# Kernel tuning notes

Measured on AMD Instinct MI355X. Metric: run time of the kernel, lower is better.

## Reference

```python
import jax, jax.numpy as jnp
import numpy as np

B, N, F, H, R = 16, 64, 64, 4, 50
C = F * H  # n_coefficients = n_heads * hidden_features
CUTOFF = 5.0  # ExpNormalSmearing cutoff_upper (cutoff_lower = 0)


def _dense(k, fin, fout):
    s = 1.0 / np.sqrt(fin)
    return jax.random.uniform(k, (fin, fout), jnp.float32, -s, s)


def setup_inputs() -> dict:
    key = jax.random.key(0)
    ks = jax.random.split(key, 20)
    start = float(np.exp(-CUTOFF))
    return {
        "h": jax.random.normal(ks[0], (B, N, F), jnp.float32),
        "x": jax.random.normal(ks[1], (B, N, 3), jnp.float32),
        "v": jax.random.normal(ks[2], (B, N, 3), jnp.float32) * 0.1,
        # edge model (ContinuousFilterConvolutionWithConcatenation)
        "W_in": _dense(ks[3], 2 * F, R), "b_in": jnp.zeros((R,), jnp.float32),
        "rbf_means": jnp.linspace(start, 1.0, R).astype(jnp.float32),
        "rbf_betas": jnp.full((R,), (2.0 / R * (1.0 - start)) ** -2, jnp.float32),
        "W_e1": _dense(ks[4], 2 * F + R + 1, F), "b_e1": jnp.zeros((F,), jnp.float32),
        "W_e2": _dense(ks[5], F, F), "b_e2": jnp.zeros((F,), jnp.float32),
        # semantic attention
        "W_sem": _dense(ks[6], F, H), "b_sem": jnp.zeros((H,), jnp.float32),
        "log_gamma": -jnp.log(jnp.linspace(1.0, 5.0, H)).astype(jnp.float32),
        # spatial attention
        "W_xmix": _dense(ks[7], C, C),
        "W_post1": _dense(ks[8], C, F), "b_post1": jnp.zeros((F,), jnp.float32),
        "W_post2": _dense(ks[9], F, F), "b_post2": jnp.zeros((F,), jnp.float32),
        # node update
        "W_node1": _dense(ks[10], F + C + F, F), "b_node1": jnp.zeros((F,), jnp.float32),
        "W_node2": _dense(ks[11], F, F), "b_node2": jnp.zeros((F,), jnp.float32),
        # velocity update
        "W_vel1": _dense(ks[12], F, F), "b_vel1": jnp.zeros((F,), jnp.float32),
        "W_vel2": _dense(ks[13], F, 1),
        "W_vmix": _dense(ks[14], C, 1),
    }


def reference(h, x, v, W_in, b_in, rbf_means, rbf_betas, W_e1, b_e1, W_e2, b_e2,
              W_sem, b_sem, log_gamma, W_xmix, W_post1, b_post1, W_post2, b_post2,
              W_node1, b_node1, W_node2, b_node2, W_vel1, b_vel1, W_vel2, W_vmix):
    silu = jax.nn.silu
    n = h.shape[-2]
    # pairwise displacement x_j - x_i : (B, N, N, 3)
    x_minus_xt = x[..., None, :, :] - x[..., :, None, :]
    d = jnp.sqrt(jax.nn.relu((x_minus_xt ** 2).sum(-1, keepdims=True)) + 1e-5)  # (B,N,N,1)
    # pairwise node features [h_j, h_i] : (B, N, N, 2F)
    hj = jnp.broadcast_to(h[..., None, :, :], h.shape[:-2] + (n, n, h.shape[-1]))
    hi = jnp.broadcast_to(h[..., :, None, :], hj.shape)
    h_cat = jnp.concatenate([hj, hi], -1)
    # edge model: RBF-smeared continuous-filter conv with concatenation
    h_mid = h_cat @ W_in + b_in  # (B,N,N,R)
    cut = 0.5 * (jnp.cos(d * (jnp.pi / CUTOFF)) + 1.0) * (d < CUTOFF)
    rbf = cut * jnp.exp(-rbf_betas * (jnp.exp(-d) - rbf_means) ** 2)  # (B,N,N,R)
    h_e = jnp.concatenate([h_cat, rbf * h_mid, d], -1)
    h_e = silu(h_e @ W_e1 + b_e1) @ W_e2 + b_e2  # (B,N,N,F)
    # attentions, softmax over neighbor axis (-2), diagonal masked out
    eye = jnp.eye(n, dtype=h.dtype)[:, :, None]
    sem = jax.nn.celu(h_e @ W_sem + b_sem, alpha=2.0) - 1e5 * eye
    sem = jax.nn.softmax(sem, axis=-2)  # (B,N,N,H)
    euc = jax.nn.softmax(-(d + 1e5 * eye) * jnp.exp(log_gamma), axis=-2)  # (B,N,N,H)
    att = euc * sem
    att = att / att.sum(-2, keepdims=True)
    # per-head attention-weighted edge features, flattened (F outer, H inner)
    h_e_att = (h_e[..., :, None] * att[..., None, :]).reshape(att.shape[:-1] + (F * H,))
    # spatial attention on unit displacement vectors
    coeff = jnp.tanh(h_e_att @ W_xmix)  # (B,N,N,C)
    x_hat = x_minus_xt / (d + 1e-5)
    comb = x_hat[..., None, :] * coeff[..., None]  # (B,N,N,C,3)
    comb_sum = comb.mean(axis=-3)  # mean over neighbors -> (B,N,C,3)
    h_comb = (comb_sum ** 2).sum(-1)  # invariant squared norms (B,N,C)
    h_comb = silu(silu(h_comb @ W_post1 + b_post1) @ W_post2 + b_post2)
    # node update (residual)
    h_agg = h_e_att.sum(axis=-2)  # (B,N,C)
    h_out = h + silu(silu(jnp.concatenate([h, h_agg, h_comb], -1) @ W_node1 + b_node1) @ W_node2 + b_node2)
    # equivariant velocity / coordinate update
    delta_v = jnp.einsum('...ijcd,c->...id', comb, W_vmix[:, 0]) / n  # v_mixing + mean over j
    gate = 2.0 * jax.nn.sigmoid(silu(h_out @ W_vel1 + b_vel1) @ W_vel2)  # double_sigmoid, (B,N,1)
    v_out = delta_v + gate * v
    x_out = x + v_out
    return h_out, x_out, v_out
```

## Files before the change

### kernel.cpp

```cpp
#include <hip/hip_runtime.h>
#include <math.h>

#define NB 16
#define NN 64
#define NF 64
#define NH 4
#define NR 50
#define NC 256

typedef __attribute__((ext_vector_type(8))) short short8;
typedef __attribute__((ext_vector_type(4))) float f32x4;

#define WS_WE1R 0
#define WS_WE2  4096
#define WS_WX   9216
#define WS_PO1  74752
#define WS_NO1  91136
#define WS_PO2  115712
#define WS_NO2  119808
#define WS_VE1  123904
#define MID_F   64000
#define E1_F    (MID_F + 131072)
#define HAGG_F  (E1_F + 131072)
#define COMB_F  (HAGG_F + 262144)
#define BS2_F   (COMB_F + 786432)

__device__ __forceinline__ float siluf(float x) { return x / (1.f + __expf(-x)); }
__device__ __forceinline__ float tanhfast(float x) { return 1.f - 2.f / (__expf(2.f * x) + 1.f); }

__device__ __forceinline__ short f2bfs(float f) {
    __bf16 b = (__bf16)f;
    union { __bf16 b; short s; } u; u.b = b; return u.s;
}
__device__ __forceinline__ float bf1(ushort u) {
    union { unsigned u; float f; } c; c.u = ((unsigned)u) << 16; return c.f;
}
__device__ __forceinline__ float bflo(unsigned u) {
    union { unsigned u; float f; } c; c.u = u << 16; return c.f;
}
__device__ __forceinline__ float bfhi(unsigned u) {
    union { unsigned u; float f; } c; c.u = u & 0xFFFF0000u; return c.f;
}

__global__ __launch_bounds__(256)
void prep_kernel(const float* __restrict__ W_e1, const float* __restrict__ b_e1,
                 const float* __restrict__ W_e2, const float* __restrict__ b_e2,
                 const float* __restrict__ W_sem, const float* __restrict__ b_sem,
                 const float* __restrict__ W_xmix,
                 const float* __restrict__ W_post1, const float* __restrict__ W_node1,
                 const float* __restrict__ W_post2, const float* __restrict__ W_node2,
                 const float* __restrict__ W_vel1,
                 const float* __restrict__ h, const float* __restrict__ W_in,
                 const float* __restrict__ b_in,
                 short* __restrict__ wpack, float* __restrict__ mid,
                 float* __restrict__ e1, float* __restrict__ bs2)
{
    int blk = blockIdx.x, t = threadIdx.x;
    if (blk < 63) {
        int s = blk * 256 + t;
        if (s >= 16000) return;
        short8 val;
        if (s < 512) {
            int cl = s & 15, g = (s >> 4) & 3, q = s >> 6;
            int ks = q & 1, nt = q >> 1;
            int c = nt * 16 + cl, k0 = 32 * ks + 8 * g;
#pragma unroll
            for (int i = 0; i < 8; i++) {
                int kr = k0 + i;
                float f = (kr < 50) ? W_e1[(128 + kr) * NF + c] : (kr == 50 ? W_e1[178 * NF + c] : 0.f);
                val[i] = f2bfs(f);
            }
            *(short8*)(&wpack[WS_WE1R + s * 8]) = val;
        } else if (s < 1152) {
            int u = s - 512;
            int cl = u & 15, g = (u >> 4) & 3, q = u >> 6;
            int ks = q & 1, nt = q >> 1;
            int c = nt * 16 + cl, k0 = 32 * ks + 8 * g;
#pragma unroll
            for (int i = 0; i < 8; i++) {
                int k = k0 + i;
                float f;
                if (c < 64) f = W_e2[k * NF + c];
                else {
                    int cc = (c - 64) & 3;
                    f = 0.f;
                    for (int m = 0; m < 64; m++) f += W_e2[k * NF + m] * W_sem[m * NH + cc];
                }
                val[i] = f2bfs(f);
            }
            *(short8*)(&wpack[WS_WE2 + u * 8]) = val;
        } else if (s < 9344) {
            int u = s - 1152;
            int l2 = u & 63, ks = (u >> 6) & 1, hh = (u >> 7) & 3, ct = u >> 9;
            int lr2 = l2 & 15, lg2 = l2 >> 4;
            int c = ct * 16 + lr2, k0 = ks * 32 + lg2 * 8;
#pragma unroll
            for (int i = 0; i < 8; i++)
                val[i] = f2bfs(W_xmix[((k0 + i) * 4 + hh) * NC + c]);
            *(short8*)(&wpack[WS_WX + u * 8]) = val;
        } else if (s < 11392) {
            int u = s - 9344;
            int cl = u & 15, g = (u >> 4) & 3, q = u >> 6;
            int ks = q & 7, nt = q >> 3;
            int c = nt * 16 + cl, k0 = 32 * ks + 8 * g;
#pragma unroll
            for (int i = 0; i < 8; i++) val[i] = f2bfs(W_post1[(k0 + i) * NF + c]);
            *(short8*)(&wpack[WS_PO1 + u * 8]) = val;
        } else if (s < 14464) {
            int u = s - 11392;
            int cl = u & 15, g = (u >> 4) & 3, q = u >> 6;
            int ks = q % 12, nt = q / 12;
            int c = nt * 16 + cl, k0 = 32 * ks + 8 * g;
#pragma unroll
            for (int i = 0; i < 8; i++) val[i] = f2bfs(W_node1[(k0 + i) * NF + c]);
            *(short8*)(&wpack[WS_NO1 + u * 8]) = val;
        } else if (s < 14976) {
            int u = s - 14464;
            int cl = u & 15, g = (u >> 4) & 3, q = u >> 6;
            int ks = q & 1, nt = q >> 1;
            int c = nt * 16 + cl, k0 = 32 * ks + 8 * g;
#pragma unroll
            for (int i = 0; i < 8; i++) val[i] = f2bfs(W_post2[(k0 + i) * NF + c]);
            *(short8*)(&wpack[WS_PO2 + u * 8]) = val;
        } else if (s < 15488) {
            int u = s - 14976;
            int cl = u & 15, g = (u >> 4) & 3, q = u >> 6;
            int ks = q & 1, nt = q >> 1;
            int c = nt * 16 + cl, k0 = 32 * ks + 8 * g;
#pragma unroll
            for (int i = 0; i < 8; i++) val[i] = f2bfs(W_node2[(k0 + i) * NF + c]);
            *(short8*)(&wpack[WS_NO2 + u * 8]) = val;
        } else {
            int u = s - 15488;
            int cl = u & 15, g = (u >> 4) & 3, q = u >> 6;
            int ks = q & 1, nt = q >> 1;
            int c = nt * 16 + cl, k0 = 32 * ks + 8 * g;
#pragma unroll
            for (int i = 0; i < 8; i++) val[i] = f2bfs(W_vel1[(k0 + i) * NF + c]);
            *(short8*)(&wpack[WS_VE1 + u * 8]) = val;
        }
    } else if (blk == 63) {
        if (t < 4) {
            float acc = b_sem[t];
            for (int m = 0; m < 64; m++) acc += b_e2[m] * W_sem[m * NH + t];
            bs2[t] = acc;
        }
    } else {
        int node = blk - 64;
        __shared__ float s_hn[64];
        if (t < 64) s_hn[t] = h[node * NF + t];
        __syncthreads();
        if (t < 64) {
            float acc = 0.f;
#pragma unroll 8
            for (int k = 0; k < 64; k++) acc += s_hn[k] * W_e1[k * NF + t];
            e1[node * 128 + t] = acc;
        } else if (t < 128) {
            int f = t - 64;
            float acc = b_e1[f];
#pragma unroll 8
            for (int k = 0; k < 64; k++) acc += s_hn[k] * W_e1[(64 + k) * NF + f];
            e1[node * 128 + 64 + f] = acc;
        } else if (t < 178) {
            int r = t - 128;
            float acc = 0.f;
#pragma unroll 8
            for (int k = 0; k < 64; k++) acc += s_hn[k] * W_in[k * NR + r];
            mid[node * 128 + r] = acc;
        } else if (t >= 192 && t < 242) {
            int r = t - 192;
            float acc = b_in[r];
#pragma unroll 8
            for (int k = 0; k < 64; k++) acc += s_hn[k] * W_in[(64 + k) * NR + r];
            mid[node * 128 + 64 + r] = acc;
        }
    }
}

__global__ __launch_bounds__(256)
void sake_edge_kernel(
    const float* __restrict__ x,
    const float* __restrict__ mid, const float* __restrict__ e1,
    const float* __restrict__ rbf_means, const float* __restrict__ rbf_betas,
    const float* __restrict__ b_e2, const float* __restrict__ bs2,
    const float* __restrict__ log_gamma,
    const short* __restrict__ wpack,
    float* __restrict__ hagg_g, float* __restrict__ comb_g)
{
    const int bi = blockIdx.x;
    const int b  = bi >> 6;
    const int i  = bi & 63;
    const int t  = threadIdx.x;
    const int w  = t >> 6, l = t & 63, lr = l & 15, lg = l >> 4;

    __shared__ __align__(16) short s_A[16 * 64 * 8];
    __shared__ __align__(16) short s_he[64 * 72];
    __shared__ float s_xhat[256];
    __shared__ float s_att[256];
    __shared__ float s_midi[52];

    const short8* A8  = (const short8*)s_A;
    short8*       A8w = (short8*)s_A;
    const short8* We1p = (const short8*)(wpack + WS_WE1R);
    const short8* We2p = (const short8*)(wpack + WS_WE2);
    const short8* Wxp  = (const short8*)(wpack + WS_WX);

    if (t < 50) s_midi[t] = mid[(b * 64 + i) * 128 + 64 + t];
    if (t < 64) {
        int j = t;
        float dx = x[(b * NN + j) * 3 + 0] - x[(b * NN + i) * 3 + 0];
        float dy = x[(b * NN + j) * 3 + 1] - x[(b * NN + i) * 3 + 1];
        float dz = x[(b * NN + j) * 3 + 2] - x[(b * NN + i) * 3 + 2];
        float d2 = dx * dx + dy * dy + dz * dz;
        float d  = sqrtf(fmaxf(d2, 0.f) + 1e-5f);
        float inv = 1.f / (d + 1e-5f);
        s_xhat[j * 4 + 0] = dx * inv;
        s_xhat[j * 4 + 1] = dy * inv;
        s_xhat[j * 4 + 2] = dz * inv;
        s_xhat[j * 4 + 3] = d;
    }
    __syncthreads();

    const int fW = w * 16 + lr;
    const float* e1b = e1 + (size_t)b * 64 * 128;
    float e1i_v = e1b[i * 128 + 64 + fW];
    float e1v[4][4];
#pragma unroll
    for (int jt = 0; jt < 4; jt++)
#pragma unroll
        for (int r = 0; r < 4; r++)
            e1v[jt][r] = e1b[(jt * 16 + lg * 4 + r) * 128 + fW];
    float be2 = b_e2[fW];
    float gam = __expf(log_gamma[lr & 3]);
    float bsv = bs2[lr & 3];

    {
        int j = t & 63, p = t >> 6;
        float d = s_xhat[j * 4 + 3];
        float cut = 0.5f * (__cosf(d * 0.6283185307179586f) + 1.f) * (d < 5.f ? 1.f : 0.f);
        float emd = __expf(-d);
        const float* mj = mid + (size_t)(b * 64 + j) * 128;
#pragma unroll
        for (int q = 0; q < 2; q++) {
            int sl = 2 * p + q;
            short8 val;
#pragma unroll
            for (int e = 0; e < 8; e++) {
                int r = sl * 8 + e;
                float o;
                if (r < 50) {
                    float m = mj[r] + s_midi[r];
                    float df = emd - rbf_means[r];
                    o = cut * __expf(-rbf_betas[r] * df * df) * m;
                } else if (r == 50) o = d;
                else o = 0.f;
                val[e] = f2bfs(o);
            }
            A8w[sl * 64 + j] = val;
        }
    }
    __syncthreads();

    {
        f32x4 acc[4];
#pragma unroll
        for (int jt = 0; jt < 4; jt++)
#pragma unroll
            for (int r = 0; r < 4; r++) acc[jt][r] = e1v[jt][r] + e1i_v;
#pragma unroll
        for (int ks = 0; ks < 2; ks++) {
            short8 bb = We1p[(w * 2 + ks) * 64 + l];
#pragma unroll
            for (int jt = 0; jt < 4; jt++) {
                short8 aa = A8[(ks * 4 + lg) * 64 + jt * 16 + lr];
                acc[jt] = __builtin_amdgcn_mfma_f32_16x16x32_bf16(aa, bb, acc[jt], 0, 0, 0);
            }
        }
#pragma unroll
        for (int jt = 0; jt < 4; jt++)
#pragma unroll
            for (int r = 0; r < 4; r++) {
                int j = jt * 16 + lg * 4 + r;
                s_A[(((fW >> 3) + 8) * 64 + j) * 8 + (fW & 7)] = f2bfs(siluf(acc[jt][r]));
            }
        __syncthreads();
    }

    {
        f32x4 accE[4], accS[4];
#pragma unroll
        for (int jt = 0; jt < 4; jt++) {
            accE[jt][0] = 0.f; accE[jt][1] = 0.f; accE[jt][2] = 0.f; accE[jt][3] = 0.f;
            accS[jt][0] = 0.f; accS[jt][1] = 0.f; accS[jt][2] = 0.f; accS[jt][3] = 0.f;
        }
#pragma unroll
        for (int ks = 0; ks < 2; ks++) {
            short8 aa[4];
#pragma unroll
            for (int jt = 0; jt < 4; jt++) aa[jt] = A8[(8 + ks * 4 + lg) * 64 + jt * 16 + lr];
            short8 bb = We2p[(w * 2 + ks) * 64 + l];
#pragma unroll
            for (int jt = 0; jt < 4; jt++)
                accE[jt] = __builtin_amdgcn_mfma_f32_16x16x32_bf16(aa[jt], bb, accE[jt], 0, 0, 0);
            if (w == 0) {
                short8 bb2 = We2p[(8 + ks) * 64 + l];
#pragma unroll
                for (int jt = 0; jt < 4; jt++)
                    accS[jt] = __builtin_amdgcn_mfma_f32_16x16x32_bf16(aa[jt], bb2, accS[jt], 0, 0, 0);
            }
        }
#pragma unroll
        for (int jt = 0; jt < 4; jt++)
#pragma unroll
            for (int r = 0; r < 4; r++) {
                int j = jt * 16 + lg * 4 + r;
                s_he[j * 72 + fW] = f2bfs(accE[jt][r] + be2);
            }
        if (w == 0) {
            float cel[4][4], dj[4][4];
            float m1 = -1e30f, m2 = -1e30f;
#pragma unroll
            for (int jt = 0; jt < 4; jt++)
#pragma unroll
                for (int r = 0; r < 4; r++) {
                    int j = jt * 16 + lg * 4 + r;
                    float s = accS[jt][r] + bsv;
                    float c = fmaxf(s, 0.f) + fminf(0.f, 2.f * (__expf(0.5f * s) - 1.f));
                    float d = s_xhat[j * 4 + 3];
                    if (j == i) { c -= 1e5f; d += 1e5f; }
                    cel[jt][r] = c; dj[jt][r] = d;
                    m1 = fmaxf(m1, c);
                    m2 = fmaxf(m2, -d * gam);
                }
            m1 = fmaxf(m1, __shfl_xor(m1, 16)); m1 = fmaxf(m1, __shfl_xor(m1, 32));
            m2 = fmaxf(m2, __shfl_xor(m2, 16)); m2 = fmaxf(m2, __shfl_xor(m2, 32));
            float S1 = 0.f, S2 = 0.f;
#pragma unroll
            for (int jt = 0; jt < 4; jt++)
#pragma unroll
                for (int r = 0; r < 4; r++) {
                    float ev1 = __expf(cel[jt][r] - m1);
                    float ev2 = __expf(-dj[jt][r] * gam - m2);
                    cel[jt][r] = ev1; dj[jt][r] = ev2;
                    S1 += ev1; S2 += ev2;
                }
            S1 += __shfl_xor(S1, 16); S1 += __shfl_xor(S1, 32);
            S2 += __shfl_xor(S2, 16); S2 += __shfl_xor(S2, 32);
            float inv12 = 1.f / (S1 * S2);
            float at[4][4];
            float S3 = 0.f;
#pragma unroll
            for (int jt = 0; jt < 4; jt++)
#pragma unroll
                for (int r = 0; r < 4; r++) {
                    at[jt][r] = cel[jt][r] * dj[jt][r] * inv12;
                    S3 += at[jt][r];
                }
            S3 += __shfl_xor(S3, 16); S3 += __shfl_xor(S3, 32);
            float inv3 = 1.f / S3;
            if (lr < 4) {
#pragma unroll
                for (int jt = 0; jt < 4; jt++)
#pragma unroll
                    for (int r = 0; r < 4; r++) {
                        int j = jt * 16 + lg * 4 + r;
                        s_att[j * 4 + lr] = at[jt][r] * inv3;
                    }
            }
        }
        __syncthreads();
    }

    {
        int f2 = t >> 3, hh = (t >> 1) & 3, jh = t & 1;
        float a0 = 0.f, a1 = 0.f;
#pragma unroll 8
        for (int jj = 0; jj < 32; jj++) {
            int j = jh * 32 + jj;
            float at = s_att[j * 4 + hh];
            unsigned u = *(const unsigned*)(s_he + j * 72 + 2 * f2);
            a0 += bflo(u) * at;
            a1 += bfhi(u) * at;
        }
        a0 += __shfl_xor(a0, 1);
        a1 += __shfl_xor(a1, 1);
        if (!jh) {
            hagg_g[bi * 256 + (2 * f2) * 4 + hh]     = a0;
            hagg_g[bi * 256 + (2 * f2 + 1) * 4 + hh] = a1;
        }
    }

    {
        f32x4 acc[4][4];
#pragma unroll
        for (int jt = 0; jt < 4; jt++)
#pragma unroll
            for (int ct = 0; ct < 4; ct++) {
                acc[jt][ct][0] = 0.f; acc[jt][ct][1] = 0.f;
                acc[jt][ct][2] = 0.f; acc[jt][ct][3] = 0.f;
            }
#pragma unroll 1
        for (int h = 0; h < 4; h++) {
            float ah[4];
#pragma unroll
            for (int jt = 0; jt < 4; jt++) ah[jt] = s_att[(jt * 16 + lr) * 4 + h];
#pragma unroll
            for (int ks = 0; ks < 2; ks++) {
                short8 fr[4];
#pragma unroll
                for (int jt = 0; jt < 4; jt++) {
                    short8 he8 = *(const short8*)(s_he + (jt * 16 + lr) * 72 + ks * 32 + lg * 8);
                    short8 v;
#pragma unroll
                    for (int e = 0; e < 8; e++) v[e] = f2bfs(bf1((ushort)he8[e]) * ah[jt]);
                    fr[jt] = v;
                }
#pragma unroll
                for (int ct = 0; ct < 4; ct++) {
                    short8 bb = Wxp[(((w * 4 + ct) * 4 + h) * 2 + ks) * 64 + l];
#pragma unroll
                    for (int jt = 0; jt < 4; jt++)
                        acc[jt][ct] = __builtin_amdgcn_mfma_f32_16x16x32_bf16(fr[jt], bb, acc[jt][ct], 0, 0, 0);
                }
            }
        }
        float* cgb = comb_g + bi * 768;
#pragma unroll
        for (int ct = 0; ct < 4; ct++) {
            float p0 = 0.f, p1 = 0.f, p2 = 0.f;
#pragma unroll
            for (int jt = 0; jt < 4; jt++)
#pragma unroll
                for (int r = 0; r < 4; r++) {
                    int j = jt * 16 + lg * 4 + r;
                    float4 xh = *(const float4*)(s_xhat + j * 4);
                    float th = tanhfast(acc[jt][ct][r]);
                    p0 += xh.x * th;
                    p1 += xh.y * th;
                    p2 += xh.z * th;
                }
            p0 += __shfl_xor(p0, 16); p0 += __shfl_xor(p0, 32);
            p1 += __shfl_xor(p1, 16); p1 += __shfl_xor(p1, 32);
            p2 += __shfl_xor(p2, 16); p2 += __shfl_xor(p2, 32);
            if (lg == 0) {
                int c = (w * 4 + ct) * 16 + lr;
                cgb[c]       = p0 * (1.f / 64.f);
                cgb[256 + c] = p1 * (1.f / 64.f);
                cgb[512 + c] = p2 * (1.f / 64.f);
            }
        }
    }
}

__global__ __launch_bounds__(256)
void sake_tail_kernel(
    const float* __restrict__ h, const float* __restrict__ x, const float* __restrict__ v,
    const float* __restrict__ hagg_g, const float* __restrict__ comb_g,
    const float* __restrict__ b_post1, const float* __restrict__ b_post2,
    const float* __restrict__ b_node1, const float* __restrict__ b_node2,
    const float* __restrict__ b_vel1,
    const float* __restrict__ W_vel2, const float* __restrict__ W_vmix,
    const short* __restrict__ wpack,
    float* __restrict__ out_h, float* __restrict__ out_x, float* __restrict__ out_v)
{
    const int g0 = blockIdx.x * 16;
    const int t = threadIdx.x;
    const int w = t >> 6, l = t & 63, lr = l & 15, lg = l >> 4;

    __shared__ __align__(16) short s_Aa[88 * 16 * 8];
    __shared__ float s_wv[256];
    __shared__ float s_wv2[64];
    __shared__ float s_red[4][16];

    const short8* A8  = (const short8*)s_Aa;
    const short8* PO1p = (const short8*)(wpack + WS_PO1);
    const short8* NO1p = (const short8*)(wpack + WS_NO1);
    const short8* PO2p = (const short8*)(wpack + WS_PO2);
    const short8* NO2p = (const short8*)(wpack + WS_NO2);
    const short8* VE1p = (const short8*)(wpack + WS_VE1);

    {
        s_wv[t] = W_vmix[t];
        if (t < 64) s_wv2[t] = W_vel2[t];
        int n = t & 15, c0 = (t >> 4) * 16;
        const float* cg = comb_g + (g0 + n) * 768;
        const float* ha = hagg_g + (g0 + n) * 256;
#pragma unroll
        for (int cc = 0; cc < 16; cc++) {
            int c = c0 + cc;
            float v0 = cg[c], v1 = cg[256 + c], v2 = cg[512 + c];
            float hcp = v0 * v0 + v1 * v1 + v2 * v2;
            s_Aa[((c >> 3) * 16 + n) * 8 + (c & 7)] = f2bfs(hcp);
            s_Aa[((40 + (c >> 3)) * 16 + n) * 8 + (c & 7)] = f2bfs(ha[c]);
        }
        int f0 = (t >> 4) * 4;
#pragma unroll
        for (int ff = 0; ff < 4; ff++) {
            int f = f0 + ff;
            s_Aa[((32 + (f >> 3)) * 16 + n) * 8 + (f & 7)] = f2bfs(h[(g0 + n) * 64 + f]);
        }
    }
    __syncthreads();

    {
        f32x4 acc = {0.f, 0.f, 0.f, 0.f};
#pragma unroll
        for (int ks = 0; ks < 8; ks++) {
            short8 aa = A8[(ks * 4 + lg) * 16 + lr];
            short8 bb = PO1p[((w * 8 + ks) * 4 + lg) * 16 + lr];
            acc = __builtin_amdgcn_mfma_f32_16x16x32_bf16(aa, bb, acc, 0, 0, 0);
        }
        int f = w * 16 + lr;
        float bp = b_post1[f];
        __syncthreads();
#pragma unroll
        for (int r = 0; r < 4; r++) {
            int n = lg * 4 + r;
            s_Aa[((80 + (f >> 3)) * 16 + n) * 8 + (f & 7)] = f2bfs(siluf(acc[r] + bp));
        }
        __syncthreads();
    }
    {
        f32x4 acc = {0.f, 0.f, 0.f, 0.f};
#pragma unroll
        for (int ks = 0; ks < 2; ks++) {
            short8 aa = A8[((80 + ks * 4 + lg)) * 16 + lr];
            short8 bb = PO2p[((w * 2 + ks) * 4 + lg) * 16 + lr];
            acc = __builtin_amdgcn_mfma_f32_16x16x32_bf16(aa, bb, acc, 0, 0, 0);
        }
        int f = w * 16 + lr;
        float bp = b_post2[f];
#pragma unroll
        for (int r = 0; r < 4; r++) {
            int n = lg * 4 + r;
            s_Aa[((72 + (f >> 3)) * 16 + n) * 8 + (f & 7)] = f2bfs(siluf(acc[r] + bp));
        }
        __syncthreads();
    }
    {
        f32x4 acc = {0.f, 0.f, 0.f, 0.f};
#pragma unroll
        for (int ks = 0; ks < 12; ks++) {
            short8 aa = A8[((32 + ks * 4 + lg)) * 16 + lr];
            short8 bb = NO1p[((w * 12 + ks) * 4 + lg) * 16 + lr];
            acc = __builtin_amdgcn_mfma_f32_16x16x32_bf16(aa, bb, acc, 0, 0, 0);
        }
        int f = w * 16 + lr;
        float bp = b_node1[f];
#pragma unroll
        for (int r = 0; r < 4; r++) {
            int n = lg * 4 + r;
            s_Aa[((f >> 3) * 16 + n) * 8 + (f & 7)] = f2bfs(siluf(acc[r] + bp));
        }
        __syncthreads();
    }
    {
        f32x4 acc = {0.f, 0.f, 0.f, 0.f};
#pragma unroll
        for (int ks = 0; ks < 2; ks++) {
            short8 aa = A8[(ks * 4 + lg) * 16 + lr];
            short8 bb = NO2p[((w * 2 + ks) * 4 + lg) * 16 + lr];
            acc = __builtin_amdgcn_mfma_f32_16x16x32_bf16(aa, bb, acc, 0, 0, 0);
        }
        int f = w * 16 + lr;
        float bp = b_node2[f];
#pragma unroll
        for (int r = 0; r < 4; r++) {
            int n = lg * 4 + r;
            float ho = h[(g0 + n) * 64 + f] + siluf(acc[r] + bp);
            out_h[(g0 + n) * 64 + f] = ho;
            s_Aa[((8 + (f >> 3)) * 16 + n) * 8 + (f & 7)] = f2bfs(ho);
        }
        __syncthreads();
    }
    {
        f32x4 acc = {0.f, 0.f, 0.f, 0.f};
#pragma unroll
        for (int ks = 0; ks < 2; ks++) {
            short8 aa = A8[((8 + ks * 4 + lg)) * 16 + lr];
            short8 bb = VE1p[((w * 2 + ks) * 4 + lg) * 16 + lr];
            acc = __builtin_amdgcn_mfma_f32_16x16x32_bf16(aa, bb, acc, 0, 0, 0);
        }
        int f = w * 16 + lr;
        float bp = b_vel1[f];
        float wv2 = s_wv2[f];
#pragma unroll
        for (int r = 0; r < 4; r++) {
            float pv = siluf(acc[r] + bp) * wv2;
            pv += __shfl_xor(pv, 1); pv += __shfl_xor(pv, 2);
            pv += __shfl_xor(pv, 4); pv += __shfl_xor(pv, 8);
            if (lr == 0) s_red[w][lg * 4 + r] = pv;
        }
        __syncthreads();
    }
    {
        int n = t >> 4, qq = t & 15;
        float p0 = 0.f, p1 = 0.f, p2 = 0.f;
        const float* cg = comb_g + (g0 + n) * 768;
#pragma unroll
        for (int cc = 0; cc < 16; cc++) {
            int c = qq * 16 + cc;
            float wv = s_wv[c];
            p0 += cg[c] * wv;
            p1 += cg[256 + c] * wv;
            p2 += cg[512 + c] * wv;
        }
        p0 += __shfl_xor(p0, 1); p0 += __shfl_xor(p0, 2); p0 += __shfl_xor(p0, 4); p0 += __shfl_xor(p0, 8);
        p1 += __shfl_xor(p1, 1); p1 += __shfl_xor(p1, 2); p1 += __shfl_xor(p1, 4); p1 += __shfl_xor(p1, 8);
        p2 += __shfl_xor(p2, 1); p2 += __shfl_xor(p2, 2); p2 += __shfl_xor(p2, 4); p2 += __shfl_xor(p2, 8);
        if (qq == 0) {
            float g = s_red[0][n] + s_red[1][n] + s_red[2][n] + s_red[3][n];
            g = 2.f / (1.f + __expf(-g));
            float dv0 = p0 + g * v[(g0 + n) * 3 + 0];
            float dv1 = p1 + g * v[(g0 + n) * 3 + 1];
            float dv2 = p2 + g * v[(g0 + n) * 3 + 2];
            out_v[(g0 + n) * 3 + 0] = dv0;
            out_v[(g0 + n) * 3 + 1] = dv1;
            out_v[(g0 + n) * 3 + 2] = dv2;
            out_x[(g0 + n) * 3 + 0] = x[(g0 + n) * 3 + 0] + dv0;
            out_x[(g0 + n) * 3 + 1] = x[(g0 + n) * 3 + 1] + dv1;
            out_x[(g0 + n) * 3 + 2] = x[(g0 + n) * 3 + 2] + dv2;
        }
    }
}

extern "C" void kernel_launch(void* const* d_in, const int* in_sizes, int n_in,
                              void* d_out, int out_size, void* d_ws, size_t ws_size,
                              hipStream_t stream) {
    const float* h        = (const float*)d_in[0];
    const float* x        = (const float*)d_in[1];
    const float* v        = (const float*)d_in[2];
    const float* W_in     = (const float*)d_in[3];
    const float* b_in     = (const float*)d_in[4];
    const float* rbf_m    = (const float*)d_in[5];
    const float* rbf_b    = (const float*)d_in[6];
    const float* W_e1     = (const float*)d_in[7];
    const float* b_e1     = (const float*)d_in[8];
    const float* W_e2     = (const float*)d_in[9];
    const float* b_e2     = (const float*)d_in[10];
    const float* W_sem    = (const float*)d_in[11];
    const float* b_sem    = (const float*)d_in[12];
    const float* log_g    = (const float*)d_in[13];
    const float* W_xmix   = (const float*)d_in[14];
    const float* W_post1  = (const float*)d_in[15];
    const float* b_post1  = (const float*)d_in[16];
    const float* W_post2  = (const float*)d_in[17];
    const float* b_post2  = (const float*)d_in[18];
    const float* W_node1  = (const float*)d_in[19];
    const float* b_node1  = (const float*)d_in[20];
    const float* W_node2  = (const float*)d_in[21];
    const float* b_node2  = (const float*)d_in[22];
    const float* W_vel1   = (const float*)d_in[23];
    const float* b_vel1   = (const float*)d_in[24];
    const float* W_vel2   = (const float*)d_in[25];
    const float* W_vmix   = (const float*)d_in[26];

    float* out   = (float*)d_out;
    float* out_h = out;
    float* out_x = out + NB * NN * NF;
    float* out_v = out + NB * NN * NF + NB * NN * 3;

    short* wpack = (short*)d_ws;
    float* wsf   = (float*)d_ws;
    float* mid   = wsf + MID_F;
    float* e1    = wsf + E1_F;
    float* hagg  = wsf + HAGG_F;
    float* comb  = wsf + COMB_F;
    float* bs2   = wsf + BS2_F;

    prep_kernel<<<64 + 1024, 256, 0, stream>>>(
        W_e1, b_e1, W_e2, b_e2, W_sem, b_sem, W_xmix,
        W_post1, W_node1, W_post2, W_node2, W_vel1,
        h, W_in, b_in, wpack, mid, e1, bs2);

    sake_edge_kernel<<<NB * NN, 256, 0, stream>>>(
        x, mid, e1, rbf_m, rbf_b, b_e2, bs2, log_g,
        wpack, hagg, comb);

    sake_tail_kernel<<<64, 256, 0, stream>>>(
        h, x, v, hagg, comb,
        b_post1, b_post2, b_node1, b_node2, b_vel1,
        W_vel2, W_vmix, wpack, out_h, out_x, out_v);
}
```

Measured before the change: 60.91 us.

## Fuse node tail MLPs into per-node edge kernel and drop tail launch

Removes the separate tail kernel and performs the post, node, and velocity MLPs per node at the end of the edge kernel. Scalar fp32 dot products read weights straight from global memory, with intermediates kept in reused shared memory. This eliminates one launch and the global round trip of the hagg and comb buffers. The prep kernel now packs fewer weights and computes four nodes per block. The cost is that every one of the 1024 blocks rereads the tail weights (about 100 KB) with scalar loads instead of 64 blocks using MFMA, which adds L2 traffic and a serial tail phase to each block.

```diff
diff --git a/kernel.cpp b/kernel.cpp
--- a/kernel.cpp
+++ b/kernel.cpp
@@ -14,16 +14,17 @@
 #define WS_WE1R 0
 #define WS_WE2  4096
 #define WS_WX   9216
-#define WS_PO1  74752
-#define WS_NO1  91136
-#define WS_PO2  115712
-#define WS_NO2  119808
-#define WS_VE1  123904
-#define MID_F   64000
+#define MID_F   40960
 #define E1_F    (MID_F + 131072)
-#define HAGG_F  (E1_F + 131072)
-#define COMB_F  (HAGG_F + 262144)
-#define BS2_F   (COMB_F + 786432)
+#define BS2_F   (E1_F + 131072)
+
+#define SP_COMB 0
+#define SP_HCP  768
+#define SP_IN   1024
+#define SP_RED  1408
+#define SP_VEC  1664
+#define SP_HO   1728
+#define SP_MISC 1792
 
 __device__ __forceinline__ float siluf(float x) { return x / (1.f + __expf(-x)); }
 __device__ __forceinline__ float tanhfast(float x) { return 1.f - 2.f / (__expf(2.f * x) + 1.f); }
@@ -40,6 +41,11 @@
 }
 __device__ __forceinline__ float bfhi(unsigned u) {
     union { unsigned u; float f; } c; c.u = u & 0xFFFF0000u; return c.f;
+}
+__device__ __forceinline__ float wave_sum(float v) {
+#pragma unroll
+    for (int s = 32; s >= 1; s >>= 1) v += __shfl_xor(v, s);
+    return v;
 }
 
 __global__ __launch_bounds__(256)
@@ -47,18 +53,15 @@
                  const float* __restrict__ W_e2, const float* __restrict__ b_e2,
                  const float* __restrict__ W_sem, const float* __restrict__ b_sem,
                  const float* __restrict__ W_xmix,
-                 const float* __restrict__ W_post1, const float* __restrict__ W_node1,
-                 const float* __restrict__ W_post2, const float* __restrict__ W_node2,
-                 const float* __restrict__ W_vel1,
                  const float* __restrict__ h, const float* __restrict__ W_in,
                  const float* __restrict__ b_in,
                  short* __restrict__ wpack, float* __restrict__ mid,
                  float* __restrict__ e1, float* __restrict__ bs2)
 {
     int blk = blockIdx.x, t = threadIdx.x;
-    if (blk < 63) {
+    if (blk < 37) {
         int s = blk * 256 + t;
-        if (s >= 16000) return;
+        if (s >= 9344) return;
         short8 val;
         if (s < 512) {
             int cl = s & 15, g = (s >> 4) & 3, q = s >> 6;
@@ -89,7 +92,7 @@
                 val[i] = f2bfs(f);
             }
             *(short8*)(&wpack[WS_WE2 + u * 8]) = val;
-        } else if (s < 9344) {
+        } else {
             int u = s - 1152;
             int l2 = u & 63, ks = (u >> 6) & 1, hh = (u >> 7) & 3, ct = u >> 9;
             int lr2 = l2 & 15, lg2 = l2 >> 4;
@@ -98,94 +101,56 @@
             for (int i = 0; i < 8; i++)
                 val[i] = f2bfs(W_xmix[((k0 + i) * 4 + hh) * NC + c]);
             *(short8*)(&wpack[WS_WX + u * 8]) = val;
-        } else if (s < 11392) {
-            int u = s - 9344;
-            int cl = u & 15, g = (u >> 4) & 3, q = u >> 6;
-            int ks = q & 7, nt = q >> 3;
-            int c = nt * 16 + cl, k0 = 32 * ks + 8 * g;
-#pragma unroll
-            for (int i = 0; i < 8; i++) val[i] = f2bfs(W_post1[(k0 + i) * NF + c]);
-            *(short8*)(&wpack[WS_PO1 + u * 8]) = val;
-        } else if (s < 14464) {
-            int u = s - 11392;
-            int cl = u & 15, g = (u >> 4) & 3, q = u >> 6;
-            int ks = q % 12, nt = q / 12;
-            int c = nt * 16 + cl, k0 = 32 * ks + 8 * g;
-#pragma unroll
-            for (int i = 0; i < 8; i++) val[i] = f2bfs(W_node1[(k0 + i) * NF + c]);
-            *(short8*)(&wpack[WS_NO1 + u * 8]) = val;
-        } else if (s < 14976) {
-            int u = s - 14464;
-            int cl = u & 15, g = (u >> 4) & 3, q = u >> 6;
-            int ks = q & 1, nt = q >> 1;
-            int c = nt * 16 + cl, k0 = 32 * ks + 8 * g;
-#pragma unroll
-            for (int i = 0; i < 8; i++) val[i] = f2bfs(W_post2[(k0 + i) * NF + c]);
-            *(short8*)(&wpack[WS_PO2 + u * 8]) = val;
-        } else if (s < 15488) {
-            int u = s - 14976;
-            int cl = u & 15, g = (u >> 4) & 3, q = u >> 6;
-            int ks = q & 1, nt = q >> 1;
-            int c = nt * 16 + cl, k0 = 32 * ks + 8 * g;
-#pragma unroll
-            for (int i = 0; i < 8; i++) val[i] = f2bfs(W_node2[(k0 + i) * NF + c]);
-            *(short8*)(&wpack[WS_NO2 + u * 8]) = val;
-        } else {
-            int u = s - 15488;
-            int cl = u & 15, g = (u >> 4) & 3, q = u >> 6;
-            int ks = q & 1, nt = q >> 1;
-            int c = nt * 16 + cl, k0 = 32 * ks + 8 * g;
-#pragma unroll
-            for (int i = 0; i < 8; i++) val[i] = f2bfs(W_vel1[(k0 + i) * NF + c]);
-            *(short8*)(&wpack[WS_VE1 + u * 8]) = val;
-        }
-    } else if (blk == 63) {
+        }
+    } else if (blk == 37) {
         if (t < 4) {
             float acc = b_sem[t];
             for (int m = 0; m < 64; m++) acc += b_e2[m] * W_sem[m * NH + t];
             bs2[t] = acc;
         }
     } else {
-        int node = blk - 64;
-        __shared__ float s_hn[64];
-        if (t < 64) s_hn[t] = h[node * NF + t];
-        __syncthreads();
-        if (t < 64) {
-            float acc = 0.f;
-#pragma unroll 8
-            for (int k = 0; k < 64; k++) acc += s_hn[k] * W_e1[k * NF + t];
-            e1[node * 128 + t] = acc;
-        } else if (t < 128) {
-            int f = t - 64;
-            float acc = b_e1[f];
-#pragma unroll 8
-            for (int k = 0; k < 64; k++) acc += s_hn[k] * W_e1[(64 + k) * NF + f];
-            e1[node * 128 + 64 + f] = acc;
-        } else if (t < 178) {
-            int r = t - 128;
-            float acc = 0.f;
-#pragma unroll 8
-            for (int k = 0; k < 64; k++) acc += s_hn[k] * W_in[k * NR + r];
-            mid[node * 128 + r] = acc;
-        } else if (t >= 192 && t < 242) {
-            int r = t - 192;
-            float acc = b_in[r];
-#pragma unroll 8
-            for (int k = 0; k < 64; k++) acc += s_hn[k] * W_in[(64 + k) * NR + r];
-            mid[node * 128 + 64 + r] = acc;
+        int w = t >> 6, l = t & 63;
+        int node = (blk - 38) * 4 + w;
+        __shared__ float s_hn[4][64];
+        s_hn[w][l] = h[node * NF + l];
+        float a0 = 0.f, a1 = b_e1[l];
+#pragma unroll 8
+        for (int k = 0; k < 64; k++) {
+            float hv = s_hn[w][k];
+            a0 += hv * W_e1[k * NF + l];
+            a1 += hv * W_e1[(64 + k) * NF + l];
+        }
+        e1[node * 128 + l] = a0;
+        e1[node * 128 + 64 + l] = a1;
+        if (l < 50) {
+            float m0 = 0.f, m1 = b_in[l];
+#pragma unroll 8
+            for (int k = 0; k < 64; k++) {
+                float hv = s_hn[w][k];
+                m0 += hv * W_in[k * NR + l];
+                m1 += hv * W_in[(64 + k) * NR + l];
+            }
+            mid[node * 128 + l] = m0;
+            mid[node * 128 + 64 + l] = m1;
         }
     }
 }
 
 __global__ __launch_bounds__(256)
-void sake_edge_kernel(
-    const float* __restrict__ x,
+void sake_fused_kernel(
+    const float* __restrict__ h, const float* __restrict__ x, const float* __restrict__ vin,
     const float* __restrict__ mid, const float* __restrict__ e1,
     const float* __restrict__ rbf_means, const float* __restrict__ rbf_betas,
     const float* __restrict__ b_e2, const float* __restrict__ bs2,
     const float* __restrict__ log_gamma,
     const short* __restrict__ wpack,
-    float* __restrict__ hagg_g, float* __restrict__ comb_g)
+    const float* __restrict__ W_post1, const float* __restrict__ b_post1,
+    const float* __restrict__ W_post2, const float* __restrict__ b_post2,
+    const float* __restrict__ W_node1, const float* __restrict__ b_node1,
+    const float* __restrict__ W_node2, const float* __restrict__ b_node2,
+    const float* __restrict__ W_vel1, const float* __restrict__ b_vel1,
+    const float* __restrict__ W_vel2, const float* __restrict__ W_vmix,
+    float* __restrict__ out_h, float* __restrict__ out_x, float* __restrict__ out_v)
 {
     const int bi = blockIdx.x;
     const int b  = bi >> 6;
@@ -201,6 +166,7 @@
 
     const short8* A8  = (const short8*)s_A;
     short8*       A8w = (short8*)s_A;
+    float*        SP  = (float*)s_A;
     const short8* We1p = (const short8*)(wpack + WS_WE1R);
     const short8* We2p = (const short8*)(wpack + WS_WE2);
     const short8* Wxp  = (const short8*)(wpack + WS_WX);
@@ -372,6 +338,7 @@
     }
 
     {
+        if (t < 64) SP[SP_IN + t] = h[bi * 64 + t];
         int f2 = t >> 3, hh = (t >> 1) & 3, jh = t & 1;
         float a0 = 0.f, a1 = 0.f;
 #pragma unroll 8
@@ -385,8 +352,8 @@
         a0 += __shfl_xor(a0, 1);
         a1 += __shfl_xor(a1, 1);
         if (!jh) {
-            hagg_g[bi * 256 + (2 * f2) * 4 + hh]     = a0;
-            hagg_g[bi * 256 + (2 * f2 + 1) * 4 + hh] = a1;
+            SP[SP_IN + 64 + (2 * f2) * 4 + hh]     = a0;
+            SP[SP_IN + 64 + (2 * f2 + 1) * 4 + hh] = a1;
         }
     }
 
@@ -400,31 +367,30 @@
                 acc[jt][ct][2] = 0.f; acc[jt][ct][3] = 0.f;
             }
 #pragma unroll 1
-        for (int h = 0; h < 4; h++) {
+        for (int hh = 0; hh < 4; hh++) {
             float ah[4];
 #pragma unroll
-            for (int jt = 0; jt < 4; jt++) ah[jt] = s_att[(jt * 16 + lr) * 4 + h];
+            for (int jt = 0; jt < 4; jt++) ah[jt] = s_att[(jt * 16 + lr) * 4 + hh];
 #pragma unroll
             for (int ks = 0; ks < 2; ks++) {
                 short8 fr[4];
 #pragma unroll
                 for (int jt = 0; jt < 4; jt++) {
                     short8 he8 = *(const short8*)(s_he + (jt * 16 + lr) * 72 + ks * 32 + lg * 8);
-                    short8 v;
-#pragma unroll
-                    for (int e = 0; e < 8; e++) v[e] = f2bfs(bf1((ushort)he8[e]) * ah[jt]);
-                    fr[jt] = v;
+                    short8 vv;
+#pragma unroll
+                    for (int e = 0; e < 8; e++) vv[e] = f2bfs(bf1((ushort)he8[e]) * ah[jt]);
+                    fr[jt] = vv;
                 }
 #pragma unroll
                 for (int ct = 0; ct < 4; ct++) {
-                    short8 bb = Wxp[(((w * 4 + ct) * 4 + h) * 2 + ks) * 64 + l];
+                    short8 bb = Wxp[(((w * 4 + ct) * 4 + hh) * 2 + ks) * 64 + l];
 #pragma unroll
                     for (int jt = 0; jt < 4; jt++)
                         acc[jt][ct] = __builtin_amdgcn_mfma_f32_16x16x32_bf16(fr[jt], bb, acc[jt][ct], 0, 0, 0);
                 }
             }
         }
-        float* cgb = comb_g + bi * 768;
 #pragma unroll
         for (int ct = 0; ct < 4; ct++) {
             float p0 = 0.f, p1 = 0.f, p2 = 0.f;
@@ -444,183 +410,86 @@
             p2 += __shfl_xor(p2, 16); p2 += __shfl_xor(p2, 32);
             if (lg == 0) {
                 int c = (w * 4 + ct) * 16 + lr;
-                cgb[c]       = p0 * (1.f / 64.f);
-                cgb[256 + c] = p1 * (1.f / 64.f);
-                cgb[512 + c] = p2 * (1.f / 64.f);
-            }
-        }
-    }
-}
-
-__global__ __launch_bounds__(256)
-void sake_tail_kernel(
-    const float* __restrict__ h, const float* __restrict__ x, const float* __restrict__ v,
-    const float* __restrict__ hagg_g, const float* __restrict__ comb_g,
-    const float* __restrict__ b_post1, const float* __restrict__ b_post2,
-    const float* __restrict__ b_node1, const float* __restrict__ b_node2,
-    const float* __restrict__ b_vel1,
-    const float* __restrict__ W_vel2, const float* __restrict__ W_vmix,
-    const short* __restrict__ wpack,
-    float* __restrict__ out_h, float* __restrict__ out_x, float* __restrict__ out_v)
-{
-    const int g0 = blockIdx.x * 16;
-    const int t = threadIdx.x;
-    const int w = t >> 6, l = t & 63, lr = l & 15, lg = l >> 4;
-
-    __shared__ __align__(16) short s_Aa[88 * 16 * 8];
-    __shared__ float s_wv[256];
-    __shared__ float s_wv2[64];
-    __shared__ float s_red[4][16];
-
-    const short8* A8  = (const short8*)s_Aa;
-    const short8* PO1p = (const short8*)(wpack + WS_PO1);
-    const short8* NO1p = (const short8*)(wpack + WS_NO1);
-    const short8* PO2p = (const short8*)(wpack + WS_PO2);
-    const short8* NO2p = (const short8*)(wpack + WS_NO2);
-    const short8* VE1p = (const short8*)(wpack + WS_VE1);
-
-    {
-        s_wv[t] = W_vmix[t];
-        if (t < 64) s_wv2[t] = W_vel2[t];
-        int n = t & 15, c0 = (t >> 4) * 16;
-        const float* cg = comb_g + (g0 + n) * 768;
-        const float* ha = hagg_g + (g0 + n) * 256;
-#pragma unroll
-        for (int cc = 0; cc < 16; cc++) {
-            int c = c0 + cc;
-            float v0 = cg[c], v1 = cg[256 + c], v2 = cg[512 + c];
-            float hcp = v0 * v0 + v1 * v1 + v2 * v2;
-            s_Aa[((c >> 3) * 16 + n) * 8 + (c & 7)] = f2bfs(hcp);
-            s_Aa[((40 + (c >> 3)) * 16 + n) * 8 + (c & 7)] = f2bfs(ha[c]);
-        }
-        int f0 = (t >> 4) * 4;
-#pragma unroll
-        for (int ff = 0; ff < 4; ff++) {
-            int f = f0 + ff;
-            s_Aa[((32 + (f >> 3)) * 16 + n) * 8 + (f & 7)] = f2bfs(h[(g0 + n) * 64 + f]);
-        }
-    }
-    __syncthreads();
-
-    {
-        f32x4 acc = {0.f, 0.f, 0.f, 0.f};
-#pragma unroll
-        for (int ks = 0; ks < 8; ks++) {
-            short8 aa = A8[(ks * 4 + lg) * 16 + lr];
-            short8 bb = PO1p[((w * 8 + ks) * 4 + lg) * 16 + lr];
-            acc = __builtin_amdgcn_mfma_f32_16x16x32_bf16(aa, bb, acc, 0, 0, 0);
-        }
-        int f = w * 16 + lr;
-        float bp = b_post1[f];
-        __syncthreads();
-#pragma unroll
-        for (int r = 0; r < 4; r++) {
-            int n = lg * 4 + r;
-            s_Aa[((80 + (f >> 3)) * 16 + n) * 8 + (f & 7)] = f2bfs(siluf(acc[r] + bp));
-        }
-        __syncthreads();
-    }
-    {
-        f32x4 acc = {0.f, 0.f, 0.f, 0.f};
-#pragma unroll
-        for (int ks = 0; ks < 2; ks++) {
-            short8 aa = A8[((80 + ks * 4 + lg)) * 16 + lr];
-            short8 bb = PO2p[((w * 2 + ks) * 4 + lg) * 16 + lr];
-            acc = __builtin_amdgcn_mfma_f32_16x16x32_bf16(aa, bb, acc, 0, 0, 0);
-        }
-        int f = w * 16 + lr;
-        float bp = b_post2[f];
-#pragma unroll
-        for (int r = 0; r < 4; r++) {
-            int n = lg * 4 + r;
-            s_Aa[((72 + (f >> 3)) * 16 + n) * 8 + (f & 7)] = f2bfs(siluf(acc[r] + bp));
-        }
-        __syncthreads();
-    }
-    {
-        f32x4 acc = {0.f, 0.f, 0.f, 0.f};
-#pragma unroll
-        for (int ks = 0; ks < 12; ks++) {
-            short8 aa = A8[((32 + ks * 4 + lg)) * 16 + lr];
-            short8 bb = NO1p[((w * 12 + ks) * 4 + lg) * 16 + lr];
-            acc = __builtin_amdgcn_mfma_f32_16x16x32_bf16(aa, bb, acc, 0, 0, 0);
-        }
-        int f = w * 16 + lr;
-        float bp = b_node1[f];
-#pragma unroll
-        for (int r = 0; r < 4; r++) {
-            int n = lg * 4 + r;
-            s_Aa[((f >> 3) * 16 + n) * 8 + (f & 7)] = f2bfs(siluf(acc[r] + bp));
-        }
-        __syncthreads();
-    }
-    {
-        f32x4 acc = {0.f, 0.f, 0.f, 0.f};
-#pragma unroll
-        for (int ks = 0; ks < 2; ks++) {
-            short8 aa = A8[(ks * 4 + lg) * 16 + lr];
-            short8 bb = NO2p[((w * 2 + ks) * 4 + lg) * 16 + lr];
-            acc = __builtin_amdgcn_mfma_f32_16x16x32_bf16(aa, bb, acc, 0, 0, 0);
-        }
-        int f = w * 16 + lr;
-        float bp = b_node2[f];
-#pragma unroll
-        for (int r = 0; r < 4; r++) {
-            int n = lg * 4 + r;
-            float ho = h[(g0 + n) * 64 + f] + siluf(acc[r] + bp);
-            out_h[(g0 + n) * 64 + f] = ho;
-            s_Aa[((8 + (f >> 3)) * 16 + n) * 8 + (f & 7)] = f2bfs(ho);
-        }
-        __syncthreads();
-    }
-    {
-        f32x4 acc = {0.f, 0.f, 0.f, 0.f};
-#pragma unroll
-        for (int ks = 0; ks < 2; ks++) {
-            short8 aa = A8[((8 + ks * 4 + lg)) * 16 + lr];
-            short8 bb = VE1p[((w * 2 + ks) * 4 + lg) * 16 + lr];
-            acc = __builtin_amdgcn_mfma_f32_16x16x32_bf16(aa, bb, acc, 0, 0, 0);
-        }
-        int f = w * 16 + lr;
-        float bp = b_vel1[f];
-        float wv2 = s_wv2[f];
-#pragma unroll
-        for (int r = 0; r < 4; r++) {
-            float pv = siluf(acc[r] + bp) * wv2;
-            pv += __shfl_xor(pv, 1); pv += __shfl_xor(pv, 2);
-            pv += __shfl_xor(pv, 4); pv += __shfl_xor(pv, 8);
-            if (lr == 0) s_red[w][lg * 4 + r] = pv;
-        }
-        __syncthreads();
-    }
-    {
-        int n = t >> 4, qq = t & 15;
-        float p0 = 0.f, p1 = 0.f, p2 = 0.f;
-        const float* cg = comb_g + (g0 + n) * 768;
-#pragma unroll
-        for (int cc = 0; cc < 16; cc++) {
-            int c = qq * 16 + cc;
-            float wv = s_wv[c];
-            p0 += cg[c] * wv;
-            p1 += cg[256 + c] * wv;
-            p2 += cg[512 + c] * wv;
-        }
-        p0 += __shfl_xor(p0, 1); p0 += __shfl_xor(p0, 2); p0 += __shfl_xor(p0, 4); p0 += __shfl_xor(p0, 8);
-        p1 += __shfl_xor(p1, 1); p1 += __shfl_xor(p1, 2); p1 += __shfl_xor(p1, 4); p1 += __shfl_xor(p1, 8);
-        p2 += __shfl_xor(p2, 1); p2 += __shfl_xor(p2, 2); p2 += __shfl_xor(p2, 4); p2 += __shfl_xor(p2, 8);
-        if (qq == 0) {
-            float g = s_red[0][n] + s_red[1][n] + s_red[2][n] + s_red[3][n];
-            g = 2.f / (1.f + __expf(-g));
-            float dv0 = p0 + g * v[(g0 + n) * 3 + 0];
-            float dv1 = p1 + g * v[(g0 + n) * 3 + 1];
-            float dv2 = p2 + g * v[(g0 + n) * 3 + 2];
-            out_v[(g0 + n) * 3 + 0] = dv0;
-            out_v[(g0 + n) * 3 + 1] = dv1;
-            out_v[(g0 + n) * 3 + 2] = dv2;
-            out_x[(g0 + n) * 3 + 0] = x[(g0 + n) * 3 + 0] + dv0;
-            out_x[(g0 + n) * 3 + 1] = x[(g0 + n) * 3 + 1] + dv1;
-            out_x[(g0 + n) * 3 + 2] = x[(g0 + n) * 3 + 2] + dv2;
-        }
+                float c0 = p0 * (1.f / 64.f);
+                float c1 = p1 * (1.f / 64.f);
+                float c2 = p2 * (1.f / 64.f);
+                SP[SP_COMB + c]       = c0;
+                SP[SP_COMB + 256 + c] = c1;
+                SP[SP_COMB + 512 + c] = c2;
+                SP[SP_HCP + c] = c0 * c0 + c1 * c1 + c2 * c2;
+            }
+        }
+    }
+    __syncthreads();
+
+    const int f = l;
+    {
+        float p = 0.f;
+#pragma unroll 8
+        for (int k = w * 64; k < w * 64 + 64; k++) p += SP[SP_HCP + k] * W_post1[k * NF + f];
+        SP[SP_RED + w * 64 + f] = p;
+    }
+    __syncthreads();
+    if (w == 0) {
+        float a = b_post1[f] + SP[SP_RED + f] + SP[SP_RED + 64 + f]
+                + SP[SP_RED + 128 + f] + SP[SP_RED + 192 + f];
+        SP[SP_VEC + f] = siluf(a);
+    }
+    __syncthreads();
+    {
+        float a = b_post2[f];
+#pragma unroll 8
+        for (int k = 0; k < 64; k++) a += SP[SP_VEC + k] * W_post2[k * NF + f];
+        if (w == 0) SP[SP_IN + 320 + f] = siluf(a);
+    }
+    __syncthreads();
+    {
+        float p = 0.f;
+#pragma unroll 8
+        for (int k = w * 96; k < w * 96 + 96; k++) p += SP[SP_IN + k] * W_node1[k * NF + f];
+        SP[SP_RED + w * 64 + f] = p;
+    }
+    __syncthreads();
+    if (w == 0) {
+        float a = b_node1[f] + SP[SP_RED + f] + SP[SP_RED + 64 + f]
+                + SP[SP_RED + 128 + f] + SP[SP_RED + 192 + f];
+        SP[SP_VEC + f] = siluf(a);
+    }
+    __syncthreads();
+    {
+        float a = b_node2[f];
+#pragma unroll 8
+        for (int k = 0; k < 64; k++) a += SP[SP_VEC + k] * W_node2[k * NF + f];
+        if (w == 0) {
+            float ho = SP[SP_IN + f] + siluf(a);
+            out_h[bi * NF + f] = ho;
+            SP[SP_HO + f] = ho;
+        }
+    }
+    __syncthreads();
+    {
+        if (w == 0) {
+            float a = b_vel1[f];
+#pragma unroll 8
+            for (int k = 0; k < 64; k++) a += SP[SP_HO + k] * W_vel1[k * NF + f];
+            float pv = siluf(a) * W_vel2[f];
+            float g = wave_sum(pv);
+            if (f == 0) SP[SP_MISC + 0] = 2.f / (1.f + __expf(-g));
+        } else {
+            int k3 = w - 1;
+            float p = 0.f;
+#pragma unroll
+            for (int q = 0; q < 4; q++)
+                p += SP[SP_COMB + k3 * 256 + q * 64 + f] * W_vmix[q * 64 + f];
+            float dv = wave_sum(p);
+            if (f == 0) SP[SP_MISC + w] = dv;
+        }
+    }
+    __syncthreads();
+    if (t < 3) {
+        float vout = SP[SP_MISC + 1 + t] + SP[SP_MISC + 0] * vin[bi * 3 + t];
+        out_v[bi * 3 + t] = vout;
+        out_x[bi * 3 + t] = x[bi * 3 + t] + vout;
     }
 }
 
@@ -664,21 +533,15 @@
     float* wsf   = (float*)d_ws;
     float* mid   = wsf + MID_F;
     float* e1    = wsf + E1_F;
-    float* hagg  = wsf + HAGG_F;
-    float* comb  = wsf + COMB_F;
     float* bs2   = wsf + BS2_F;
 
-    prep_kernel<<<64 + 1024, 256, 0, stream>>>(
+    prep_kernel<<<38 + 256, 256, 0, stream>>>(
         W_e1, b_e1, W_e2, b_e2, W_sem, b_sem, W_xmix,
-        W_post1, W_node1, W_post2, W_node2, W_vel1,
         h, W_in, b_in, wpack, mid, e1, bs2);
 
-    sake_edge_kernel<<<NB * NN, 256, 0, stream>>>(
-        x, mid, e1, rbf_m, rbf_b, b_e2, bs2, log_g,
-        wpack, hagg, comb);
-
-    sake_tail_kernel<<<64, 256, 0, stream>>>(
-        h, x, v, hagg, comb,
-        b_post1, b_post2, b_node1, b_node2, b_vel1,
-        W_vel2, W_vmix, wpack, out_h, out_x, out_v);
-}
+    sake_fused_kernel<<<NB * NN, 256, 0, stream>>>(
+        h, x, v, mid, e1, rbf_m, rbf_b, b_e2, bs2, log_g, wpack,
+        W_post1, b_post1, W_post2, b_post2, W_node1, b_node1,
+        W_node2, b_node2, W_vel1, b_vel1, W_vel2, W_vmix,
+        out_h, out_x, out_v);
+}
```

Result: slower. 67.96 us (+11.6%).
